# Optimization experiments

Measured on AMD Instinct MI355X. Metric: run time of the kernel, lower is better.

## Reference

```python
import jax, jax.numpy as jnp
import numpy as np

D_MODEL = 512
N_HEADS = 8
HEAD_SIZE = 64


def setup_inputs() -> dict:
    key = jax.random.key(0)
    ks = jax.random.split(key, 6)
    B, T = 4, 2048
    x_q = jax.random.normal(ks[0], (B, T, D_MODEL), dtype=jnp.float32)
    s = 1.0 / np.sqrt(D_MODEL)
    # per-head q/k/v projection weights, stacked: [H, head_size, d_model]
    Wq = jax.random.normal(ks[1], (N_HEADS, HEAD_SIZE, D_MODEL), dtype=jnp.float32) * s
    Wk = jax.random.normal(ks[2], (N_HEADS, HEAD_SIZE, D_MODEL), dtype=jnp.float32) * s
    Wv = jax.random.normal(ks[3], (N_HEADS, HEAD_SIZE, D_MODEL), dtype=jnp.float32) * s
    Wp = jax.random.normal(ks[4], (D_MODEL, D_MODEL), dtype=jnp.float32) * s
    bp = jax.random.normal(ks[5], (D_MODEL,), dtype=jnp.float32) * 0.01
    return {"x_q": x_q, "Wq": Wq, "Wk": Wk, "Wv": Wv, "Wp": Wp, "bp": bp}


def reference(x_q, Wq, Wk, Wv, Wp, bp):
    B, T, C = x_q.shape  # C == d_model
    # per-head projections: [B, H, T, K]
    q = jnp.einsum('btd,hkd->bhtk', x_q, Wq)
    k = jnp.einsum('btd,hkd->bhtk', x_q, Wk)
    v = jnp.einsum('btd,hkd->bhtk', x_q, Wv)
    # NOTE: original scales by C**-0.5 with C = d_model (not head_size)
    scores = jnp.einsum('bhtk,bhsk->bhts', q, k) * (C ** -0.5)
    causal = jnp.tril(jnp.ones((T, T), dtype=bool))
    scores = jnp.where(causal, scores, -jnp.inf)
    wei = jax.nn.softmax(scores, axis=-1)  # dropout is identity in eval
    out = jnp.einsum('bhts,bhsk->bhtk', wei, v)
    # concat heads: [B, T, H*K] == [B, T, d_model]
    out = out.transpose(0, 2, 1, 3).reshape(B, T, C)
    return out @ Wp.T + bp
```

## Files before the change

kernel.cpp:

```cpp
#include <hip/hip_runtime.h>
#include <hip/hip_bf16.h>

using bf16x8 = __attribute__((ext_vector_type(8))) __bf16;
using f32x4  = __attribute__((ext_vector_type(4))) float;
using f32x16 = __attribute__((ext_vector_type(16))) float;
using i32x4  = __attribute__((ext_vector_type(4))) int;

#define MFMA_16x16x32(a, b, c) __builtin_amdgcn_mfma_f32_16x16x32_bf16((a), (b), (c), 0, 0, 0)
#define MFMA32(a, b, c)        __builtin_amdgcn_mfma_f32_32x32x16_bf16((a), (b), (c), 0, 0, 0)

#define GLOAD16(g, l)                                                         \
    __builtin_amdgcn_global_load_lds(                                         \
        (const __attribute__((address_space(1))) unsigned int*)(g),           \
        (__attribute__((address_space(3))) unsigned int*)(l), 16, 0, 0)

__device__ __forceinline__ ushort f2bf(float f) {
    return __builtin_bit_cast(ushort, (__bf16)f);
}
__device__ __forceinline__ unsigned pk_bf16(float lo, float hi) {
    unsigned r;
    asm volatile("v_cvt_pk_bf16_f32 %0, %1, %2" : "=v"(r) : "v"(lo), "v"(hi));
    return r;
}
__device__ __forceinline__ void pl32_swap(unsigned &a, unsigned &b) {
    asm volatile("v_permlane32_swap_b32 %0, %1" : "+v"(a), "+v"(b));
}

__global__ __launch_bounds__(256) void cvt_bf16(
    const float* __restrict__ in, ushort* __restrict__ out, int n)
{
    const int i = (blockIdx.x * 256 + threadIdx.x) * 8;
    if (i + 8 <= n) {
        const f32x4 a = *(const f32x4*)(in + i);
        const f32x4 b = *(const f32x4*)(in + i + 4);
        union { ushort u[8]; i32x4 w; } p;
        #pragma unroll
        for (int j = 0; j < 4; ++j) { p.u[j] = f2bf(a[j]); p.u[4 + j] = f2bf(b[j]); }
        *(i32x4*)(out + i) = p.w;
    }
}

__global__ __launch_bounds__(256) void cvt_w3(
    const float* __restrict__ w0, const float* __restrict__ w1,
    const float* __restrict__ w2, ushort* __restrict__ out)
{
    const int i = (blockIdx.x * 256 + threadIdx.x) * 8;
    const int w = i >> 18, off = i & 262143;
    const float* src = (w == 0) ? w0 : ((w == 1) ? w1 : w2);
    const f32x4 a = *(const f32x4*)(src + off);
    const f32x4 b = *(const f32x4*)(src + off + 4);
    union { ushort u[8]; i32x4 v; } p;
    #pragma unroll
    for (int j = 0; j < 4; ++j) { p.u[j] = f2bf(a[j]); p.u[4 + j] = f2bf(b[j]); }
    *(i32x4*)(out + i) = p.v;
}

__global__ __launch_bounds__(256) void gemm_qkv3(
    const ushort* __restrict__ A, const ushort* __restrict__ Wbf,
    float qscale, ushort* __restrict__ qb, ushort* __restrict__ kb,
    ushort* __restrict__ vb)
{
    __shared__ ushort lA[2][128][32];
    __shared__ ushort lB[2][128][32];
    const int wsel = blockIdx.y >> 2;
    const int n0 = (blockIdx.y & 3) * 128;
    const ushort* W = Wbf + wsel * 262144;
    ushort* out = (wsel == 0) ? qb : ((wsel == 1) ? kb : vb);
    const float scale = (wsel == 0) ? qscale : 1.0f;

    const int m0 = blockIdx.x * 128;
    const int tid  = threadIdx.x;
    const int lane = tid & 63;
    const int wave = tid >> 6;
    const int wr = (wave >> 1) * 64, wc = (wave & 1) * 64;
    const int frow = lane & 15;
    const int fkp  = (((lane >> 4) ^ ((lane >> 1) & 3))) * 8;

    const int srw  = lane >> 2;
    const int scol = ((lane & 3) ^ ((lane >> 3) & 3)) * 8;

    f32x4 acc[4][4] = {};
    auto stage = [&](int k0, int b) {
        #pragma unroll
        for (int i = 0; i < 2; ++i) {
            const int rb = (wave * 2 + i) * 16;
            GLOAD16(A + (size_t)(m0 + rb + srw) * 512 + k0 + scol, &lA[b][rb][0]);
            GLOAD16(W + (size_t)(n0 + rb + srw) * 512 + k0 + scol, &lB[b][rb][0]);
        }
    };

    stage(0, 0);
    for (int t = 0; t < 16; ++t) {
        const int p = t & 1;
        __syncthreads();
        if (t + 1 < 16) stage((t + 1) * 32, p ^ 1);

        bf16x8 af[4], bg[4];
        #pragma unroll
        for (int m = 0; m < 4; ++m) af[m] = *(const bf16x8*)&lA[p][wr + m * 16 + frow][fkp];
        #pragma unroll
        for (int n = 0; n < 4; ++n) bg[n] = *(const bf16x8*)&lB[p][wc + n * 16 + frow][fkp];
        #pragma unroll
        for (int m = 0; m < 4; ++m)
            #pragma unroll
            for (int n = 0; n < 4; ++n)
                acc[m][n] = MFMA_16x16x32(af[m], bg[n], acc[m][n]);
    }

    const int rbase = (lane >> 4) * 4;
    const int ccol  = lane & 15;
    if (wsel == 2) {
        #pragma unroll
        for (int m = 0; m < 4; ++m)
            #pragma unroll
            for (int n = 0; n < 4; ++n) {
                const int col = n0 + wc + n * 16 + ccol;
                const int row0 = m0 + wr + m * 16 + rbase;
                unsigned long long u = 0;
                #pragma unroll
                for (int r = 0; r < 4; ++r)
                    u |= ((unsigned long long)f2bf(acc[m][n][r])) << (16 * r);
                const size_t idx = ((size_t)((row0 >> 11) * 8 + (col >> 6)) * 64
                                    + (col & 63)) * 2048 + (row0 & 2047);
                *(unsigned long long*)(out + idx) = u;
            }
    } else {
        #pragma unroll
        for (int m = 0; m < 4; ++m)
            #pragma unroll
            for (int n = 0; n < 4; ++n) {
                const int col = n0 + wc + n * 16 + ccol;
                #pragma unroll
                for (int r = 0; r < 4; ++r) {
                    const int row = m0 + wr + m * 16 + rbase + r;
                    out[(((row >> 11) * 8 + (col >> 6)) * 2048 + (row & 2047)) * 64 + (col & 63)]
                        = f2bf(acc[m][n][r] * scale);
                }
            }
    }
}

__global__ __launch_bounds__(256) void gemm_out(
    const ushort* __restrict__ A, const float* __restrict__ W,
    const float* __restrict__ bias, float* __restrict__ out)
{
    __shared__ ushort lA[128][40];
    __shared__ ushort lB[128][40];
    const int m0 = blockIdx.x * 128;
    const int n0 = blockIdx.y * 128;
    const int tid  = threadIdx.x;
    const int lane = tid & 63;
    const int wave = tid >> 6;
    const int wr = (wave >> 1) * 64, wc = (wave & 1) * 64;
    const int frow = lane & 15, fk = (lane >> 4) * 8;
    const int sr = tid >> 1, scc = (tid & 1) * 16;

    f32x4 acc[4][4] = {};
    i32x4 va0, va1;
    f32x4 b0, b1, b2, b3;
    auto load = [&](int k0) {
        const int row = m0 + sr, c = k0 + scc;
        const ushort* pa = A + ((((row >> 11) * 8 + (c >> 6)) * 2048 + (row & 2047)) * 64 + (c & 63));
        va0 = *(const i32x4*)(pa);
        va1 = *(const i32x4*)(pa + 8);
        const float* pb = W + (n0 + sr) * 512 + k0 + scc;
        b0 = *(const f32x4*)(pb);
        b1 = *(const f32x4*)(pb + 4);
        b2 = *(const f32x4*)(pb + 8);
        b3 = *(const f32x4*)(pb + 12);
    };

    load(0);
    for (int t = 0; t < 16; ++t) {
        union { ushort u[16]; i32x4 w[2]; } pB;
        #pragma unroll
        for (int j = 0; j < 4; ++j) {
            pB.u[j]      = f2bf(b0[j]);  pB.u[4 + j]  = f2bf(b1[j]);
            pB.u[8 + j]  = f2bf(b2[j]);  pB.u[12 + j] = f2bf(b3[j]);
        }
        __syncthreads();
        *(i32x4*)&lA[sr][scc]     = va0;
        *(i32x4*)&lA[sr][scc + 8] = va1;
        *(i32x4*)&lB[sr][scc]     = pB.w[0];
        *(i32x4*)&lB[sr][scc + 8] = pB.w[1];
        if (t + 1 < 16) load((t + 1) * 32);
        __syncthreads();

        bf16x8 af[4], bg[4];
        #pragma unroll
        for (int m = 0; m < 4; ++m) af[m] = *(const bf16x8*)&lA[wr + m * 16 + frow][fk];
        #pragma unroll
        for (int n = 0; n < 4; ++n) bg[n] = *(const bf16x8*)&lB[wc + n * 16 + frow][fk];
        #pragma unroll
        for (int m = 0; m < 4; ++m)
            #pragma unroll
            for (int n = 0; n < 4; ++n)
                acc[m][n] = MFMA_16x16x32(af[m], bg[n], acc[m][n]);
    }

    const int rbase = (lane >> 4) * 4;
    const int ccol  = lane & 15;
    #pragma unroll
    for (int m = 0; m < 4; ++m)
        #pragma unroll
        for (int n = 0; n < 4; ++n) {
            const int col = n0 + wc + n * 16 + ccol;
            const float bv = bias[col];
            #pragma unroll
            for (int r = 0; r < 4; ++r) {
                const int row = m0 + wr + m * 16 + rbase + r;
                out[row * 512 + col] = acc[m][n][r] + bv;
            }
        }
}

__global__ __launch_bounds__(256, 2) void attn_kernel(
    const ushort* __restrict__ q, const ushort* __restrict__ k,
    const ushort* __restrict__ vt, ushort* __restrict__ att)
{
    __shared__ ushort lK[2][64][64];
    __shared__ ushort lV[2][64][64];

    const int NB   = (int)(gridDim.x * gridDim.y);
    const int NH   = NB >> 4;
    const int half = NB >> 1;
    const int n    = (int)(blockIdx.y * gridDim.x + blockIdx.x);
    const int r    = (n < half) ? n : (NB - 1 - (n - half));
    const int qt0  = (15 - r / NH) * 128;
    const int bh   = r % NH;

    const ushort* Q  = q  + (size_t)bh * 2048 * 64;
    const ushort* K  = k  + (size_t)bh * 2048 * 64;
    const ushort* VT = vt + (size_t)bh * 2048 * 64;
    ushort* O = att + (size_t)bh * 2048 * 64;

    const int tid = threadIdx.x;
    const int wv  = tid >> 6;
    const int l   = tid & 63;
    const int ql  = l & 31;
    const int hi  = l >> 5;
    const int wrow0 = qt0 + wv * 32;
    const int qrow  = wrow0 + ql;
    const int wmax  = wrow0 + 31;
    const int qkey  = ql & 7;
    const float LOG2E = 1.44269504088896f;

    const int srow = tid >> 2;
    const int sg   = (tid & 3) * 2;
    const int skey = srow & 7;

    bf16x8 aq[4];
    #pragma unroll
    for (int kk = 0; kk < 4; ++kk)
        aq[kk] = *(const bf16x8*)(Q + (size_t)qrow * 64 + kk * 16 + hi * 8);

    f32x16 o0 = {}, o1 = {};
    float mrun = -30000.0f, lrun = 0.0f;
    const int nt = qt0 / 64 + 2;

    i32x4 kr0, kr1, vr0, vr1;
    auto loadG = [&](int s0) {
        const ushort* kp = K + (size_t)(s0 + srow) * 64 + (tid & 3) * 16;
        kr0 = *(const i32x4*)(kp);
        kr1 = *(const i32x4*)(kp + 8);
        const ushort* vp = VT + (size_t)srow * 2048 + s0 + (tid & 3) * 16;
        vr0 = *(const i32x4*)(vp);
        vr1 = *(const i32x4*)(vp + 8);
    };
    auto writeL = [&](int b) {
        *(i32x4*)&lK[b][srow][((sg    ) ^ skey) * 8] = kr0;
        *(i32x4*)&lK[b][srow][((sg + 1) ^ skey) * 8] = kr1;
        *(i32x4*)&lV[b][srow][((sg    ) ^ skey) * 8] = vr0;
        *(i32x4*)&lV[b][srow][((sg + 1) ^ skey) * 8] = vr1;
    };

    loadG(0);
    writeL(0);
    if (nt > 1) loadG(64);

    for (int t = 0; t < nt; ++t) {
        const int p  = t & 1;
        const int s0 = t * 64;
        __syncthreads();
        if (t + 1 < nt) writeL(p ^ 1);
        if (t + 2 < nt) loadG(s0 + 128);

        if (s0 > wmax) continue;

        f32x16 sa = {}, sb = {};
        #pragma unroll
        for (int kk = 0; kk < 4; ++kk) {
            const bf16x8 kb0 = *(const bf16x8*)&lK[p][ql]     [((2 * kk + hi) ^ qkey) * 8];
            const bf16x8 kb1 = *(const bf16x8*)&lK[p][32 + ql][((2 * kk + hi) ^ qkey) * 8];
            sa = MFMA32(kb0, aq[kk], sa);
            sb = MFMA32(kb1, aq[kk], sb);
        }

        if (s0 + 63 > wrow0) {
            #pragma unroll
            for (int rr = 0; rr < 16; ++rr) {
                const int cr = (rr & 3) + 8 * (rr >> 2) + 4 * hi;
                if (s0 + cr > qrow)      sa[rr] = -30000.0f;
                if (s0 + 32 + cr > qrow) sb[rr] = -30000.0f;
            }
        }

        float tm[16];
        #pragma unroll
        for (int rr = 0; rr < 16; ++rr) tm[rr] = fmaxf(sa[rr], sb[rr]);
        #pragma unroll
        for (int s = 8; s > 0; s >>= 1)
            #pragma unroll
            for (int rr = 0; rr < s; ++rr) tm[rr] = fmaxf(tm[rr], tm[rr + s]);
        float pmax = fmaxf(tm[0], __shfl_xor(tm[0], 32));

        if (__any(pmax > mrun + 8.0f)) {
            const float mnew  = fmaxf(mrun, pmax);
            const float alpha = exp2f((mrun - mnew) * LOG2E);
            mrun = mnew;
            lrun *= alpha;
            #pragma unroll
            for (int rr = 0; rr < 16; ++rr) {
                const float ar = __shfl(alpha, (rr & 3) + 8 * (rr >> 2) + 4 * hi);
                o0[rr] *= ar; o1[rr] *= ar;
            }
        }

        const float mb = mrun * LOG2E;
        #pragma unroll
        for (int rr = 0; rr < 16; ++rr) {
            sa[rr] = exp2f(fmaf(sa[rr], LOG2E, -mb));
            sb[rr] = exp2f(fmaf(sb[rr], LOG2E, -mb));
        }
        float tu[16];
        #pragma unroll
        for (int rr = 0; rr < 16; ++rr) tu[rr] = sa[rr] + sb[rr];
        #pragma unroll
        for (int s = 8; s > 0; s >>= 1)
            #pragma unroll
            for (int rr = 0; rr < s; ++rr) tu[rr] += tu[rr + s];
        lrun += tu[0] + __shfl_xor(tu[0], 32);

        unsigned paw[4][4];
        #pragma unroll
        for (int ks = 0; ks < 4; ++ks) {
            const int e = 2 * ks, f = 2 * ks + 1;
            const int ra = 4 * (e & 3), rb = 4 * (f & 3);
            unsigned A0, A1, B0, B1;
            if (e >> 2) { A0 = pk_bf16(sb[ra], sb[ra + 1]); A1 = pk_bf16(sb[ra + 2], sb[ra + 3]); }
            else        { A0 = pk_bf16(sa[ra], sa[ra + 1]); A1 = pk_bf16(sa[ra + 2], sa[ra + 3]); }
            if (f >> 2) { B0 = pk_bf16(sb[rb], sb[rb + 1]); B1 = pk_bf16(sb[rb + 2], sb[rb + 3]); }
            else        { B0 = pk_bf16(sa[rb], sa[rb + 1]); B1 = pk_bf16(sa[rb + 2], sa[rb + 3]); }
            pl32_swap(A0, B0);
            pl32_swap(A1, B1);
            paw[ks][0] = A0; paw[ks][1] = A1; paw[ks][2] = B0; paw[ks][3] = B1;
        }

        #pragma unroll
        for (int ks = 0; ks < 4; ++ks) {
            union { unsigned w[4]; bf16x8 v; } u;
            u.w[0] = paw[ks][0]; u.w[1] = paw[ks][1];
            u.w[2] = paw[ks][2]; u.w[3] = paw[ks][3];
            const bf16x8 v0 = *(const bf16x8*)&lV[p][ql]     [((2 * ks + hi) ^ qkey) * 8];
            const bf16x8 v1 = *(const bf16x8*)&lV[p][32 + ql][((2 * ks + hi) ^ qkey) * 8];
            o0 = MFMA32(u.v, v0, o0);
            o1 = MFMA32(u.v, v1, o1);
        }
    }

    const float linv = 1.0f / fmaxf(lrun, 1e-30f);
    #pragma unroll
    for (int rr = 0; rr < 16; ++rr) {
        const int cr = (rr & 3) + 8 * (rr >> 2) + 4 * hi;
        const float li = __shfl(linv, cr);
        const int row = wrow0 + cr;
        O[(size_t)row * 64 + ql]      = f2bf(o0[rr] * li);
        O[(size_t)row * 64 + 32 + ql] = f2bf(o1[rr] * li);
    }
}

extern "C" void kernel_launch(void* const* d_in, const int* in_sizes, int n_in,
                              void* d_out, int out_size, void* d_ws, size_t ws_size,
                              hipStream_t stream) {
    const float* x  = (const float*)d_in[0];
    const float* Wq = (const float*)d_in[1];
    const float* Wk = (const float*)d_in[2];
    const float* Wv = (const float*)d_in[3];
    const float* Wp = (const float*)d_in[4];
    const float* bp = (const float*)d_in[5];
    float* out = (float*)d_out;

    const size_t NEL  = 4u * 8u * 2048u * 64u;
    const size_t NELB = 8u * 2048u * 64u;
    const float qscale = 0.04419417382415922f;

    if (ws_size >= 3u * NEL * sizeof(ushort)) {
        ushort* xbf = (ushort*)d_out;
        ushort* qb  = xbf + NEL;
        ushort* kb  = (ushort*)d_ws;
        ushort* vb  = kb + NEL;
        ushort* ab  = vb + NEL;
        ushort* wbf = ab;
        hipLaunchKernelGGL(cvt_bf16, dim3((int)(NEL / (256 * 8))), dim3(256), 0, stream,
                           x, xbf, (int)NEL);
        hipLaunchKernelGGL(cvt_w3, dim3(384), dim3(256), 0, stream, Wq, Wk, Wv, wbf);
        hipLaunchKernelGGL(gemm_qkv3, dim3(64, 12), dim3(256), 0, stream,
                           xbf, wbf, qscale, qb, kb, vb);
        hipLaunchKernelGGL(attn_kernel, dim3(16, 32), dim3(256), 0, stream, qb, kb, vb, ab);
        hipLaunchKernelGGL(gemm_out, dim3(64, 4), dim3(256), 0, stream, ab, Wp, bp, out);
    } else {
        ushort* kb = (ushort*)d_ws;
        ushort* vb = kb + NELB;
        ushort* ab = vb + NELB;
        ushort* wbf = ab;
        for (int b = 0; b < 4; ++b) {
            const float* xb = x + (size_t)b * 2048u * 512u;
            float* ob = out + (size_t)b * 2048u * 512u;
            ushort* xbf = (ushort*)ob;
            ushort* qb  = xbf + NELB;
            hipLaunchKernelGGL(cvt_bf16, dim3((int)(NELB / (256 * 8))), dim3(256), 0, stream,
                               xb, xbf, (int)NELB);
            hipLaunchKernelGGL(cvt_w3, dim3(384), dim3(256), 0, stream, Wq, Wk, Wv, wbf);
            hipLaunchKernelGGL(gemm_qkv3, dim3(16, 12), dim3(256), 0, stream,
                               xbf, wbf, qscale, qb, kb, vb);
            hipLaunchKernelGGL(attn_kernel, dim3(16, 8), dim3(256), 0, stream, qb, kb, vb, ab);
            hipLaunchKernelGGL(gemm_out, dim3(16, 4), dim3(256), 0, stream, ab, Wp, bp, ob);
        }
    }
}
```

Before: 104.1 us.

## Double-buffer output GEMM via direct LDS loads and widen attention KV staging

The output projection now reads a bf16 copy of Wp, produced by an extra conversion launch. It stages A and W tiles straight into double-buffered, swizzled shared memory with async global-to-LDS loads. This removes the per-iteration register staging, fp32-to-bf16 conversion and one barrier. The attention kernel loads 128 keys per synchronization step (two 64-key halves) to halve barrier count, at the cost of more shared memory and registers and possibly lower occupancy. The extra Wp conversion kernel adds a launch.

```diff
diff --git a/kernel.cpp b/kernel.cpp
--- a/kernel.cpp
+++ b/kernel.cpp
@@ -141,56 +141,47 @@
 }
 
 __global__ __launch_bounds__(256) void gemm_out(
-    const ushort* __restrict__ A, const float* __restrict__ W,
+    const ushort* __restrict__ A, const ushort* __restrict__ W,
     const float* __restrict__ bias, float* __restrict__ out)
 {
-    __shared__ ushort lA[128][40];
-    __shared__ ushort lB[128][40];
+    __shared__ ushort lA[2][128][32];
+    __shared__ ushort lB[2][128][32];
     const int m0 = blockIdx.x * 128;
     const int n0 = blockIdx.y * 128;
     const int tid  = threadIdx.x;
     const int lane = tid & 63;
     const int wave = tid >> 6;
     const int wr = (wave >> 1) * 64, wc = (wave & 1) * 64;
-    const int frow = lane & 15, fk = (lane >> 4) * 8;
-    const int sr = tid >> 1, scc = (tid & 1) * 16;
+    const int frow = lane & 15;
+    const int fkp  = (((lane >> 4) ^ ((lane >> 1) & 3))) * 8;
+
+    const int srw  = lane >> 2;
+    const int scol = ((lane & 3) ^ ((lane >> 3) & 3)) * 8;
 
     f32x4 acc[4][4] = {};
-    i32x4 va0, va1;
-    f32x4 b0, b1, b2, b3;
-    auto load = [&](int k0) {
-        const int row = m0 + sr, c = k0 + scc;
-        const ushort* pa = A + ((((row >> 11) * 8 + (c >> 6)) * 2048 + (row & 2047)) * 64 + (c & 63));
-        va0 = *(const i32x4*)(pa);
-        va1 = *(const i32x4*)(pa + 8);
-        const float* pb = W + (n0 + sr) * 512 + k0 + scc;
-        b0 = *(const f32x4*)(pb);
-        b1 = *(const f32x4*)(pb + 4);
-        b2 = *(const f32x4*)(pb + 8);
-        b3 = *(const f32x4*)(pb + 12);
+    auto stage = [&](int k0, int b) {
+        #pragma unroll
+        for (int i = 0; i < 2; ++i) {
+            const int rb = (wave * 2 + i) * 16;
+            const int row = m0 + rb + srw, c = k0 + scol;
+            const size_t ia = (((size_t)(row >> 11) * 8 + (c >> 6)) * 2048
+                               + (row & 2047)) * 64 + (c & 63);
+            GLOAD16(A + ia, &lA[b][rb][0]);
+            GLOAD16(W + (size_t)(n0 + rb + srw) * 512 + k0 + scol, &lB[b][rb][0]);
+        }
     };
 
-    load(0);
+    stage(0, 0);
     for (int t = 0; t < 16; ++t) {
-        union { ushort u[16]; i32x4 w[2]; } pB;
-        #pragma unroll
-        for (int j = 0; j < 4; ++j) {
-            pB.u[j]      = f2bf(b0[j]);  pB.u[4 + j]  = f2bf(b1[j]);
-            pB.u[8 + j]  = f2bf(b2[j]);  pB.u[12 + j] = f2bf(b3[j]);
-        }
+        const int p = t & 1;
         __syncthreads();
-        *(i32x4*)&lA[sr][scc]     = va0;
-        *(i32x4*)&lA[sr][scc + 8] = va1;
-        *(i32x4*)&lB[sr][scc]     = pB.w[0];
-        *(i32x4*)&lB[sr][scc + 8] = pB.w[1];
-        if (t + 1 < 16) load((t + 1) * 32);
-        __syncthreads();
+        if (t + 1 < 16) stage((t + 1) * 32, p ^ 1);
 
         bf16x8 af[4], bg[4];
         #pragma unroll
-        for (int m = 0; m < 4; ++m) af[m] = *(const bf16x8*)&lA[wr + m * 16 + frow][fk];
-        #pragma unroll
-        for (int n = 0; n < 4; ++n) bg[n] = *(const bf16x8*)&lB[wc + n * 16 + frow][fk];
+        for (int m = 0; m < 4; ++m) af[m] = *(const bf16x8*)&lA[p][wr + m * 16 + frow][fkp];
+        #pragma unroll
+        for (int n = 0; n < 4; ++n) bg[n] = *(const bf16x8*)&lB[p][wc + n * 16 + frow][fkp];
         #pragma unroll
         for (int m = 0; m < 4; ++m)
             #pragma unroll
@@ -218,8 +209,8 @@
     const ushort* __restrict__ q, const ushort* __restrict__ k,
     const ushort* __restrict__ vt, ushort* __restrict__ att)
 {
-    __shared__ ushort lK[2][64][64];
-    __shared__ ushort lV[2][64][64];
+    __shared__ ushort lK[2][2][64][64];
+    __shared__ ushort lV[2][2][64][64];
 
     const int NB   = (int)(gridDim.x * gridDim.y);
     const int NH   = NB >> 4;
@@ -256,115 +247,125 @@
 
     f32x16 o0 = {}, o1 = {};
     float mrun = -30000.0f, lrun = 0.0f;
-    const int nt = qt0 / 64 + 2;
-
-    i32x4 kr0, kr1, vr0, vr1;
+    const int nt2 = qt0 / 128 + 1;
+
+    i32x4 kr[2][2], vr[2][2];
     auto loadG = [&](int s0) {
-        const ushort* kp = K + (size_t)(s0 + srow) * 64 + (tid & 3) * 16;
-        kr0 = *(const i32x4*)(kp);
-        kr1 = *(const i32x4*)(kp + 8);
-        const ushort* vp = VT + (size_t)srow * 2048 + s0 + (tid & 3) * 16;
-        vr0 = *(const i32x4*)(vp);
-        vr1 = *(const i32x4*)(vp + 8);
+        #pragma unroll
+        for (int hf = 0; hf < 2; ++hf) {
+            const ushort* kp = K + (size_t)(s0 + hf * 64 + srow) * 64 + (tid & 3) * 16;
+            kr[hf][0] = *(const i32x4*)(kp);
+            kr[hf][1] = *(const i32x4*)(kp + 8);
+            const ushort* vp = VT + (size_t)srow * 2048 + s0 + hf * 64 + (tid & 3) * 16;
+            vr[hf][0] = *(const i32x4*)(vp);
+            vr[hf][1] = *(const i32x4*)(vp + 8);
+        }
     };
     auto writeL = [&](int b) {
-        *(i32x4*)&lK[b][srow][((sg    ) ^ skey) * 8] = kr0;
-        *(i32x4*)&lK[b][srow][((sg + 1) ^ skey) * 8] = kr1;
-        *(i32x4*)&lV[b][srow][((sg    ) ^ skey) * 8] = vr0;
-        *(i32x4*)&lV[b][srow][((sg + 1) ^ skey) * 8] = vr1;
+        #pragma unroll
+        for (int hf = 0; hf < 2; ++hf) {
+            *(i32x4*)&lK[b][hf][srow][((sg    ) ^ skey) * 8] = kr[hf][0];
+            *(i32x4*)&lK[b][hf][srow][((sg + 1) ^ skey) * 8] = kr[hf][1];
+            *(i32x4*)&lV[b][hf][srow][((sg    ) ^ skey) * 8] = vr[hf][0];
+            *(i32x4*)&lV[b][hf][srow][((sg + 1) ^ skey) * 8] = vr[hf][1];
+        }
     };
 
     loadG(0);
     writeL(0);
-    if (nt > 1) loadG(64);
-
-    for (int t = 0; t < nt; ++t) {
-        const int p  = t & 1;
-        const int s0 = t * 64;
+    if (nt2 > 1) loadG(128);
+
+    for (int T = 0; T < nt2; ++T) {
+        const int p  = T & 1;
+        const int s0 = T * 128;
         __syncthreads();
-        if (t + 1 < nt) writeL(p ^ 1);
-        if (t + 2 < nt) loadG(s0 + 128);
-
-        if (s0 > wmax) continue;
-
-        f32x16 sa = {}, sb = {};
-        #pragma unroll
-        for (int kk = 0; kk < 4; ++kk) {
-            const bf16x8 kb0 = *(const bf16x8*)&lK[p][ql]     [((2 * kk + hi) ^ qkey) * 8];
-            const bf16x8 kb1 = *(const bf16x8*)&lK[p][32 + ql][((2 * kk + hi) ^ qkey) * 8];
-            sa = MFMA32(kb0, aq[kk], sa);
-            sb = MFMA32(kb1, aq[kk], sb);
-        }
-
-        if (s0 + 63 > wrow0) {
+        if (T + 1 < nt2) writeL(p ^ 1);
+        if (T + 2 < nt2) loadG(s0 + 256);
+
+        #pragma unroll
+        for (int hf = 0; hf < 2; ++hf) {
+            const int ss = s0 + hf * 64;
+            if (ss > wmax) continue;
+
+            f32x16 sa = {}, sb = {};
+            #pragma unroll
+            for (int kk = 0; kk < 4; ++kk) {
+                const bf16x8 kb0 = *(const bf16x8*)&lK[p][hf][ql]     [((2 * kk + hi) ^ qkey) * 8];
+                const bf16x8 kb1 = *(const bf16x8*)&lK[p][hf][32 + ql][((2 * kk + hi) ^ qkey) * 8];
+                sa = MFMA32(kb0, aq[kk], sa);
+                sb = MFMA32(kb1, aq[kk], sb);
+            }
+
+            if (ss + 63 > wrow0) {
+                #pragma unroll
+                for (int rr = 0; rr < 16; ++rr) {
+                    const int cr = (rr & 3) + 8 * (rr >> 2) + 4 * hi;
+                    if (ss + cr > qrow)      sa[rr] = -30000.0f;
+                    if (ss + 32 + cr > qrow) sb[rr] = -30000.0f;
+                }
+            }
+
+            float tm[16];
+            #pragma unroll
+            for (int rr = 0; rr < 16; ++rr) tm[rr] = fmaxf(sa[rr], sb[rr]);
+            #pragma unroll
+            for (int s = 8; s > 0; s >>= 1)
+                #pragma unroll
+                for (int rr = 0; rr < s; ++rr) tm[rr] = fmaxf(tm[rr], tm[rr + s]);
+            float pmax = fmaxf(tm[0], __shfl_xor(tm[0], 32));
+
+            if (__any(pmax > mrun + 8.0f)) {
+                const float mnew  = fmaxf(mrun, pmax);
+                const float alpha = exp2f((mrun - mnew) * LOG2E);
+                mrun = mnew;
+                lrun *= alpha;
+                #pragma unroll
+                for (int rr = 0; rr < 16; ++rr) {
+                    const float ar = __shfl(alpha, (rr & 3) + 8 * (rr >> 2) + 4 * hi);
+                    o0[rr] *= ar; o1[rr] *= ar;
+                }
+            }
+
+            const float mb = mrun * LOG2E;
             #pragma unroll
             for (int rr = 0; rr < 16; ++rr) {
-                const int cr = (rr & 3) + 8 * (rr >> 2) + 4 * hi;
-                if (s0 + cr > qrow)      sa[rr] = -30000.0f;
-                if (s0 + 32 + cr > qrow) sb[rr] = -30000.0f;
-            }
-        }
-
-        float tm[16];
-        #pragma unroll
-        for (int rr = 0; rr < 16; ++rr) tm[rr] = fmaxf(sa[rr], sb[rr]);
-        #pragma unroll
-        for (int s = 8; s > 0; s >>= 1)
-            #pragma unroll
-            for (int rr = 0; rr < s; ++rr) tm[rr] = fmaxf(tm[rr], tm[rr + s]);
-        float pmax = fmaxf(tm[0], __shfl_xor(tm[0], 32));
-
-        if (__any(pmax > mrun + 8.0f)) {
-            const float mnew  = fmaxf(mrun, pmax);
-            const float alpha = exp2f((mrun - mnew) * LOG2E);
-            mrun = mnew;
-            lrun *= alpha;
-            #pragma unroll
-            for (int rr = 0; rr < 16; ++rr) {
-                const float ar = __shfl(alpha, (rr & 3) + 8 * (rr >> 2) + 4 * hi);
-                o0[rr] *= ar; o1[rr] *= ar;
-            }
-        }
-
-        const float mb = mrun * LOG2E;
-        #pragma unroll
-        for (int rr = 0; rr < 16; ++rr) {
-            sa[rr] = exp2f(fmaf(sa[rr], LOG2E, -mb));
-            sb[rr] = exp2f(fmaf(sb[rr], LOG2E, -mb));
-        }
-        float tu[16];
-        #pragma unroll
-        for (int rr = 0; rr < 16; ++rr) tu[rr] = sa[rr] + sb[rr];
-        #pragma unroll
-        for (int s = 8; s > 0; s >>= 1)
-            #pragma unroll
-            for (int rr = 0; rr < s; ++rr) tu[rr] += tu[rr + s];
-        lrun += tu[0] + __shfl_xor(tu[0], 32);
-
-        unsigned paw[4][4];
-        #pragma unroll
-        for (int ks = 0; ks < 4; ++ks) {
-            const int e = 2 * ks, f = 2 * ks + 1;
-            const int ra = 4 * (e & 3), rb = 4 * (f & 3);
-            unsigned A0, A1, B0, B1;
-            if (e >> 2) { A0 = pk_bf16(sb[ra], sb[ra + 1]); A1 = pk_bf16(sb[ra + 2], sb[ra + 3]); }
-            else        { A0 = pk_bf16(sa[ra], sa[ra + 1]); A1 = pk_bf16(sa[ra + 2], sa[ra + 3]); }
-            if (f >> 2) { B0 = pk_bf16(sb[rb], sb[rb + 1]); B1 = pk_bf16(sb[rb + 2], sb[rb + 3]); }
-            else        { B0 = pk_bf16(sa[rb], sa[rb + 1]); B1 = pk_bf16(sa[rb + 2], sa[rb + 3]); }
-            pl32_swap(A0, B0);
-            pl32_swap(A1, B1);
-            paw[ks][0] = A0; paw[ks][1] = A1; paw[ks][2] = B0; paw[ks][3] = B1;
-        }
-
-        #pragma unroll
-        for (int ks = 0; ks < 4; ++ks) {
-            union { unsigned w[4]; bf16x8 v; } u;
-            u.w[0] = paw[ks][0]; u.w[1] = paw[ks][1];
-            u.w[2] = paw[ks][2]; u.w[3] = paw[ks][3];
-            const bf16x8 v0 = *(const bf16x8*)&lV[p][ql]     [((2 * ks + hi) ^ qkey) * 8];
-            const bf16x8 v1 = *(const bf16x8*)&lV[p][32 + ql][((2 * ks + hi) ^ qkey) * 8];
-            o0 = MFMA32(u.v, v0, o0);
-            o1 = MFMA32(u.v, v1, o1);
+                sa[rr] = exp2f(fmaf(sa[rr], LOG2E, -mb));
+                sb[rr] = exp2f(fmaf(sb[rr], LOG2E, -mb));
+            }
+            float tu[16];
+            #pragma unroll
+            for (int rr = 0; rr < 16; ++rr) tu[rr] = sa[rr] + sb[rr];
+            #pragma unroll
+            for (int s = 8; s > 0; s >>= 1)
+                #pragma unroll
+                for (int rr = 0; rr < s; ++rr) tu[rr] += tu[rr + s];
+            lrun += tu[0] + __shfl_xor(tu[0], 32);
+
+            unsigned paw[4][4];
+            #pragma unroll
+            for (int ks = 0; ks < 4; ++ks) {
+                const int e = 2 * ks, f = 2 * ks + 1;
+                const int ra = 4 * (e & 3), rb = 4 * (f & 3);
+                unsigned A0, A1, B0, B1;
+                if (e >> 2) { A0 = pk_bf16(sb[ra], sb[ra + 1]); A1 = pk_bf16(sb[ra + 2], sb[ra + 3]); }
+                else        { A0 = pk_bf16(sa[ra], sa[ra + 1]); A1 = pk_bf16(sa[ra + 2], sa[ra + 3]); }
+                if (f >> 2) { B0 = pk_bf16(sb[rb], sb[rb + 1]); B1 = pk_bf16(sb[rb + 2], sb[rb + 3]); }
+                else        { B0 = pk_bf16(sa[rb], sa[rb + 1]); B1 = pk_bf16(sa[rb + 2], sa[rb + 3]); }
+                pl32_swap(A0, B0);
+                pl32_swap(A1, B1);
+                paw[ks][0] = A0; paw[ks][1] = A1; paw[ks][2] = B0; paw[ks][3] = B1;
+            }
+
+            #pragma unroll
+            for (int ks = 0; ks < 4; ++ks) {
+                union { unsigned w[4]; bf16x8 v; } u;
+                u.w[0] = paw[ks][0]; u.w[1] = paw[ks][1];
+                u.w[2] = paw[ks][2]; u.w[3] = paw[ks][3];
+                const bf16x8 v0 = *(const bf16x8*)&lV[p][hf][ql]     [((2 * ks + hi) ^ qkey) * 8];
+                const bf16x8 v1 = *(const bf16x8*)&lV[p][hf][32 + ql][((2 * ks + hi) ^ qkey) * 8];
+                o0 = MFMA32(u.v, v0, o0);
+                o1 = MFMA32(u.v, v1, o1);
+            }
         }
     }
 
@@ -395,36 +396,40 @@
     const float qscale = 0.04419417382415922f;
 
     if (ws_size >= 3u * NEL * sizeof(ushort)) {
-        ushort* xbf = (ushort*)d_out;
-        ushort* qb  = xbf + NEL;
-        ushort* kb  = (ushort*)d_ws;
-        ushort* vb  = kb + NEL;
-        ushort* ab  = vb + NEL;
-        ushort* wbf = ab;
+        ushort* xbf  = (ushort*)d_out;
+        ushort* qb   = xbf + NEL;
+        ushort* kb   = (ushort*)d_ws;
+        ushort* vb   = kb + NEL;
+        ushort* ab   = vb + NEL;
+        ushort* wbf  = ab;
+        ushort* wpbf = kb;
         hipLaunchKernelGGL(cvt_bf16, dim3((int)(NEL / (256 * 8))), dim3(256), 0, stream,
                            x, xbf, (int)NEL);
         hipLaunchKernelGGL(cvt_w3, dim3(384), dim3(256), 0, stream, Wq, Wk, Wv, wbf);
         hipLaunchKernelGGL(gemm_qkv3, dim3(64, 12), dim3(256), 0, stream,
                            xbf, wbf, qscale, qb, kb, vb);
         hipLaunchKernelGGL(attn_kernel, dim3(16, 32), dim3(256), 0, stream, qb, kb, vb, ab);
-        hipLaunchKernelGGL(gemm_out, dim3(64, 4), dim3(256), 0, stream, ab, Wp, bp, out);
+        hipLaunchKernelGGL(cvt_bf16, dim3(128), dim3(256), 0, stream, Wp, wpbf, 262144);
+        hipLaunchKernelGGL(gemm_out, dim3(64, 4), dim3(256), 0, stream, ab, wpbf, bp, out);
     } else {
-        ushort* kb = (ushort*)d_ws;
-        ushort* vb = kb + NELB;
-        ushort* ab = vb + NELB;
+        ushort* kb  = (ushort*)d_ws;
+        ushort* vb  = kb + NELB;
+        ushort* ab  = vb + NELB;
         ushort* wbf = ab;
         for (int b = 0; b < 4; ++b) {
             const float* xb = x + (size_t)b * 2048u * 512u;
             float* ob = out + (size_t)b * 2048u * 512u;
-            ushort* xbf = (ushort*)ob;
-            ushort* qb  = xbf + NELB;
+            ushort* xbf  = (ushort*)ob;
+            ushort* qb   = xbf + NELB;
+            ushort* wpbf = kb;
             hipLaunchKernelGGL(cvt_bf16, dim3((int)(NELB / (256 * 8))), dim3(256), 0, stream,
                                xb, xbf, (int)NELB);
             hipLaunchKernelGGL(cvt_w3, dim3(384), dim3(256), 0, stream, Wq, Wk, Wv, wbf);
             hipLaunchKernelGGL(gemm_qkv3, dim3(16, 12), dim3(256), 0, stream,
                                xbf, wbf, qscale, qb, kb, vb);
             hipLaunchKernelGGL(attn_kernel, dim3(16, 8), dim3(256), 0, stream, qb, kb, vb, ab);
-            hipLaunchKernelGGL(gemm_out, dim3(16, 4), dim3(256), 0, stream, ab, Wp, bp, ob);
-        }
-    }
-}
+            hipLaunchKernelGGL(cvt_bf16, dim3(128), dim3(256), 0, stream, Wp, wpbf, 262144);
+            hipLaunchKernelGGL(gemm_out, dim3(16, 4), dim3(256), 0, stream, ab, wpbf, bp, ob);
+        }
+    }
+}
```

Result: faster. 99.20 us (-4.7%).
